# Performance work log

Measured on AMD Instinct MI355X. Metric: run time of the kernel, lower is better.

Reference implementation:

```python
import jax, jax.numpy as jnp
import numpy as np

TOP_K = 2

def setup_inputs() -> dict:
    key = jax.random.key(0)
    k1, k2, k3, k4 = jax.random.split(key, 4)
    B, S, H, E, F = 2, 1024, 1024, 16, 1024
    hidden_states = jax.random.normal(k1, (B, S, H), dtype=jnp.float32)
    router_w = jax.random.normal(k2, (H, E), dtype=jnp.float32) * 0.02
    w_gate_up = jax.random.normal(k3, (E, H, 2 * F), dtype=jnp.float32) * 0.02
    w_down = jax.random.normal(k4, (E, F, H), dtype=jnp.float32) * 0.02
    return {"hidden_states": hidden_states, "router_w": router_w,
            "w_gate_up": w_gate_up, "w_down": w_down}

def reference(hidden_states, router_w, w_gate_up, w_down):
    B, S, H = hidden_states.shape
    E = router_w.shape[-1]
    flat = hidden_states.reshape(-1, H)                      # [T, H]
    T = flat.shape[0]
    # Routing: topk_then_softmax (default softmax_order)
    logits = flat @ router_w                                 # [T, E]
    top_vals, top_idx = jax.lax.top_k(logits, TOP_K)         # [T, K]
    routing_weights = jax.nn.softmax(top_vals, axis=-1)      # [T, K]
    # Scatter routing weights into a dense combine matrix [T, E]
    combine = jnp.zeros((T, E), dtype=flat.dtype)
    combine = combine.at[jnp.arange(T)[:, None], top_idx].add(routing_weights)
    # Fused expert FFN (per _FusedExpertTemplate, act_fn = SiLU-gated)
    gu = jnp.einsum('th,ehf->etf', flat, w_gate_up)          # [E, T, 2F]
    gate, up = jnp.split(gu, 2, axis=-1)
    gated = jax.nn.silu(gate) * up                           # [E, T, F]
    expert_out = jnp.einsum('etf,efh->eth', gated, w_down)   # [E, T, H]
    out = jnp.einsum('eth,te->th', expert_out, combine)      # [T, H]
    return out.reshape(B, S, H)
```

## Files before the change

### kernel.cpp

```cpp
#include <hip/hip_runtime.h>

#define T_TOK 2048
#define H_DIM 1024
#define E_NUM 16
#define F_DIM 1024

typedef unsigned short u16;
typedef unsigned int u32;
typedef short s16x8 __attribute__((ext_vector_type(8)));
typedef float f32x4 __attribute__((ext_vector_type(4)));

__device__ __forceinline__ float b2f(u16 v) { return __uint_as_float(((u32)v) << 16); }
__device__ __forceinline__ u16 f2b(float f) {
  u32 u = __float_as_uint(f);
  return (u16)((u + 0x7fffu + ((u >> 16) & 1u)) >> 16);
}

__global__ void router_kernel(const float* __restrict__ hidden, const float* __restrict__ rw,
                              int* __restrict__ counts, int* __restrict__ routing_e,
                              float* __restrict__ routing_w) {
  int t = blockIdx.x;
  int lane = threadIdx.x;
  const float* xrow = hidden + (size_t)t * H_DIM;
  float acc[E_NUM];
#pragma unroll
  for (int e = 0; e < E_NUM; ++e) acc[e] = 0.f;
  for (int j = 0; j < H_DIM / 64; ++j) {
    int h = j * 64 + lane;
    float x = xrow[h];
    const float* wr = rw + h * E_NUM;
#pragma unroll
    for (int e = 0; e < E_NUM; ++e) acc[e] += x * wr[e];
  }
#pragma unroll
  for (int e = 0; e < E_NUM; ++e) {
    acc[e] += __shfl_xor(acc[e], 32, 64);
    acc[e] += __shfl_xor(acc[e], 16, 64);
    acc[e] += __shfl_xor(acc[e], 8, 64);
    acc[e] += __shfl_xor(acc[e], 4, 64);
    acc[e] += __shfl_xor(acc[e], 2, 64);
    acc[e] += __shfl_xor(acc[e], 1, 64);
  }
  if (lane == 0) {
    float v0 = -1e30f, v1 = -1e30f;
    int i0 = 0, i1 = 0;
#pragma unroll
    for (int e = 0; e < E_NUM; ++e) {
      float v = acc[e];
      if (v > v0) { v1 = v0; i1 = i0; v0 = v; i0 = e; }
      else if (v > v1) { v1 = v; i1 = e; }
    }
    float p0 = 1.f / (1.f + __expf(v1 - v0));
    routing_e[2 * t] = i0;
    routing_e[2 * t + 1] = i1;
    routing_w[2 * t] = p0;
    routing_w[2 * t + 1] = 1.f - p0;
    atomicAdd(&counts[i0], 1);
    atomicAdd(&counts[i1], 1);
  }
}

__global__ void scatter_kernel(const int* __restrict__ counts, int* __restrict__ offsets,
                               const int* __restrict__ routing_e, const float* __restrict__ routing_w,
                               int* __restrict__ token_of_slot, float* __restrict__ slot_w) {
  __shared__ int offs[E_NUM];
  __shared__ int cur[E_NUM];
  int tid = threadIdx.x;
  if (tid == 0) {
    int s = 0;
    for (int e = 0; e < E_NUM; ++e) { offs[e] = s; s += counts[e]; }
  }
  __syncthreads();
  if (tid < E_NUM) { offsets[tid] = offs[tid]; cur[tid] = offs[tid]; }
  __syncthreads();
  for (int i = tid; i < 2 * T_TOK; i += 256) {
    int e = routing_e[i];
    int pos = atomicAdd(&cur[e], 1);
    token_of_slot[pos] = i >> 1;
    slot_w[pos] = routing_w[i];
  }
}

struct f8v { float4 a, b; };

__device__ __forceinline__ void stage_w_pair(u32* __restrict__ B, int kp, int n0,
                                             const f8v& ev, const f8v& od) {
  const float* pe = (const float*)&ev;
  const float* po = (const float*)&od;
  int g0 = kp >> 2, w = kp & 3;
#pragma unroll
  for (int i = 0; i < 8; ++i) {
    int n = n0 + i;
    u32 word = (u32)f2b(pe[i]) | ((u32)f2b(po[i]) << 16);
    B[n * 16 + (((g0 ^ (n >> 3) ^ n) & 3) << 2) + w] = word;
  }
}

__device__ __forceinline__ s16x8 read_bfrag(const u32* __restrict__ B, int n, int q) {
  return *(const s16x8*)&B[n * 16 + (((q ^ (n >> 3) ^ n) & 3) << 2)];
}

__device__ __forceinline__ void split_pack(const float* __restrict__ p, uint4& hh, uint4& ll) {
  u16 h[8], l[8];
#pragma unroll
  for (int i = 0; i < 8; ++i) {
    h[i] = f2b(p[i]);
    l[i] = f2b(p[i] - b2f(h[i]));
  }
  hh.x = (u32)h[0] | ((u32)h[1] << 16);
  hh.y = (u32)h[2] | ((u32)h[3] << 16);
  hh.z = (u32)h[4] | ((u32)h[5] << 16);
  hh.w = (u32)h[6] | ((u32)h[7] << 16);
  ll.x = (u32)l[0] | ((u32)l[1] << 16);
  ll.y = (u32)l[2] | ((u32)l[3] << 16);
  ll.z = (u32)l[4] | ((u32)l[5] << 16);
  ll.w = (u32)l[6] | ((u32)l[7] << 16);
}

#define MFMA(a, b, c) __builtin_amdgcn_mfma_f32_16x16x32_bf16(a, b, c, 0, 0, 0)

__global__ __launch_bounds__(256, 2) void moe_gemm1(
    const float* __restrict__ hidden, const float* __restrict__ wgu,
    const int* __restrict__ token_of_slot, const int* __restrict__ counts,
    const int* __restrict__ offsets, float* __restrict__ act) {
  const int e = blockIdx.z;
  const int cnt = counts[e];
  const int m0 = blockIdx.y * 64;
  if (m0 >= cnt) return;
  const int off = offsets[e];
  const int f0 = blockIdx.x * 128;

  __shared__ u16 Xh[64][40];
  __shared__ u16 Xl[64][40];
  __shared__ u32 Bg[128 * 16];
  __shared__ u32 Bu[128 * 16];

  const int tid = threadIdx.x;
  const int lane = tid & 63;
  const int wave = tid >> 6;
  const int q = lane >> 4, ln = lane & 15;
  const int mb = (wave & 1) * 32, nb = (wave >> 1) * 64;

  const int xr = tid >> 2, xc = (tid & 3) * 8;
  const int tok = (m0 + xr < cnt) ? token_of_slot[off + m0 + xr] : 0;
  const float* xsrc = hidden + (size_t)tok * H_DIM + xc;

  const int kp = tid >> 4, n0 = (tid & 15) * 8;
  const float* wbase = wgu + (size_t)e * H_DIM * 2048;
  const float* wg0 = wbase + (size_t)(2 * kp) * 2048 + f0 + n0;
  const float* wu0 = wg0 + 1024;

  f32x4 zero = {0.f, 0.f, 0.f, 0.f};
  f32x4 accg[2][4], accu[2][4];
#pragma unroll
  for (int i = 0; i < 2; ++i)
#pragma unroll
    for (int j = 0; j < 4; ++j) { accg[i][j] = zero; accu[i][j] = zero; }

  for (int k0 = 0; k0 < H_DIM; k0 += 32) {
    float4 xa = *(const float4*)(xsrc + k0);
    float4 xb = *(const float4*)(xsrc + k0 + 4);
    size_t wofs = (size_t)k0 * 2048;
    f8v ge, go, ue, uo;
    ge.a = *(const float4*)(wg0 + wofs);
    ge.b = *(const float4*)(wg0 + wofs + 4);
    go.a = *(const float4*)(wg0 + wofs + 2048);
    go.b = *(const float4*)(wg0 + wofs + 2052);
    ue.a = *(const float4*)(wu0 + wofs);
    ue.b = *(const float4*)(wu0 + wofs + 4);
    uo.a = *(const float4*)(wu0 + wofs + 2048);
    uo.b = *(const float4*)(wu0 + wofs + 2052);
    __syncthreads();
    float xv[8] = {xa.x, xa.y, xa.z, xa.w, xb.x, xb.y, xb.z, xb.w};
    uint4 hh, ll;
    split_pack(xv, hh, ll);
    *(uint4*)&Xh[xr][xc] = hh;
    *(uint4*)&Xl[xr][xc] = ll;
    stage_w_pair(Bg, kp, n0, ge, go);
    stage_w_pair(Bu, kp, n0, ue, uo);
    __syncthreads();

    s16x8 ah[2], al[2];
    ah[0] = *(const s16x8*)&Xh[mb + ln][q * 8];
    ah[1] = *(const s16x8*)&Xh[mb + 16 + ln][q * 8];
    al[0] = *(const s16x8*)&Xl[mb + ln][q * 8];
    al[1] = *(const s16x8*)&Xl[mb + 16 + ln][q * 8];
#pragma unroll
    for (int j = 0; j < 4; ++j) {
      s16x8 bg = read_bfrag(Bg, nb + j * 16 + ln, q);
      s16x8 bu = read_bfrag(Bu, nb + j * 16 + ln, q);
#pragma unroll
      for (int i = 0; i < 2; ++i) {
        accg[i][j] = MFMA(ah[i], bg, accg[i][j]);
        accg[i][j] = MFMA(al[i], bg, accg[i][j]);
        accu[i][j] = MFMA(ah[i], bu, accu[i][j]);
        accu[i][j] = MFMA(al[i], bu, accu[i][j]);
      }
    }
  }

#pragma unroll
  for (int i = 0; i < 2; ++i) {
#pragma unroll
    for (int r = 0; r < 4; ++r) {
      int row = mb + i * 16 + q * 4 + r;
      if (m0 + row < cnt) {
        float* arow = act + (size_t)(off + m0 + row) * F_DIM + f0 + nb + ln;
#pragma unroll
        for (int j = 0; j < 4; ++j) {
          float g = accg[i][j][r], u = accu[i][j][r];
          arow[j * 16] = g * (1.f / (1.f + __expf(-g))) * u;
        }
      }
    }
  }
}

__global__ __launch_bounds__(256, 2) void moe_gemm2(
    const float* __restrict__ act, const float* __restrict__ wd,
    const int* __restrict__ token_of_slot, const float* __restrict__ slot_w,
    const int* __restrict__ counts, const int* __restrict__ offsets,
    float* __restrict__ out) {
  const int e = blockIdx.z;
  const int cnt = counts[e];
  const int m0 = blockIdx.y * 64;
  if (m0 >= cnt) return;
  const int off = offsets[e];
  const int h0 = blockIdx.x * 128;

  __shared__ u16 Ah[64][40];
  __shared__ u16 Al[64][40];
  __shared__ u32 Bd[128 * 16];

  const int tid = threadIdx.x;
  const int lane = tid & 63;
  const int wave = tid >> 6;
  const int q = lane >> 4, ln = lane & 15;
  const int mb = (wave & 1) * 32, nb = (wave >> 1) * 64;

  const int xr = tid >> 2, xc = (tid & 3) * 8;
  const int gs = (m0 + xr < cnt) ? (off + m0 + xr) : 0;
  const float* asrc = act + (size_t)gs * F_DIM + xc;

  const int kp = tid >> 4, n0 = (tid & 15) * 8;
  const float* wd0 = wd + (size_t)e * F_DIM * H_DIM + (size_t)(2 * kp) * H_DIM + h0 + n0;

  f32x4 zero = {0.f, 0.f, 0.f, 0.f};
  f32x4 acc[2][4];
#pragma unroll
  for (int i = 0; i < 2; ++i)
#pragma unroll
    for (int j = 0; j < 4; ++j) acc[i][j] = zero;

  for (int k0 = 0; k0 < F_DIM; k0 += 32) {
    float4 aa = *(const float4*)(asrc + k0);
    float4 ab = *(const float4*)(asrc + k0 + 4);
    size_t wofs = (size_t)k0 * H_DIM;
    f8v de, dd;
    de.a = *(const float4*)(wd0 + wofs);
    de.b = *(const float4*)(wd0 + wofs + 4);
    dd.a = *(const float4*)(wd0 + wofs + 1024);
    dd.b = *(const float4*)(wd0 + wofs + 1028);
    __syncthreads();
    float av[8] = {aa.x, aa.y, aa.z, aa.w, ab.x, ab.y, ab.z, ab.w};
    uint4 hh, ll;
    split_pack(av, hh, ll);
    *(uint4*)&Ah[xr][xc] = hh;
    *(uint4*)&Al[xr][xc] = ll;
    stage_w_pair(Bd, kp, n0, de, dd);
    __syncthreads();
    s16x8 ah[2], al[2];
    ah[0] = *(const s16x8*)&Ah[mb + ln][q * 8];
    ah[1] = *(const s16x8*)&Ah[mb + 16 + ln][q * 8];
    al[0] = *(const s16x8*)&Al[mb + ln][q * 8];
    al[1] = *(const s16x8*)&Al[mb + 16 + ln][q * 8];
#pragma unroll
    for (int j = 0; j < 4; ++j) {
      s16x8 bf = read_bfrag(Bd, nb + j * 16 + ln, q);
#pragma unroll
      for (int i = 0; i < 2; ++i) {
        acc[i][j] = MFMA(ah[i], bf, acc[i][j]);
        acc[i][j] = MFMA(al[i], bf, acc[i][j]);
      }
    }
  }
#pragma unroll
  for (int i = 0; i < 2; ++i) {
#pragma unroll
    for (int r = 0; r < 4; ++r) {
      int row = mb + i * 16 + q * 4 + r;
      if (m0 + row < cnt) {
        int slot = off + m0 + row;
        int tok = token_of_slot[slot];
        float wgt = slot_w[slot];
        float* orow = out + (size_t)tok * H_DIM + h0 + nb + ln;
#pragma unroll
        for (int j = 0; j < 4; ++j) atomicAdd(&orow[j * 16], wgt * acc[i][j][r]);
      }
    }
  }
}

extern "C" void kernel_launch(void* const* d_in, const int* in_sizes, int n_in,
                              void* d_out, int out_size, void* d_ws, size_t ws_size,
                              hipStream_t stream) {
  const float* hidden = (const float*)d_in[0];
  const float* rw = (const float*)d_in[1];
  const float* wgu = (const float*)d_in[2];
  const float* wd = (const float*)d_in[3];
  float* out = (float*)d_out;
  char* ws = (char*)d_ws;

  int* counts = (int*)(ws);
  int* offsets = (int*)(ws + 256);
  int* routing_e = (int*)(ws + 1024);
  float* routing_w = (float*)(ws + 17408);
  int* token_of_slot = (int*)(ws + 33792);
  float* slot_w = (float*)(ws + 50176);
  float* act = (float*)(ws + 131072);

  hipMemsetAsync(counts, 0, 64, stream);
  hipMemsetAsync(out, 0, (size_t)out_size * sizeof(float), stream);
  router_kernel<<<dim3(T_TOK), dim3(64), 0, stream>>>(hidden, rw, counts, routing_e, routing_w);
  scatter_kernel<<<dim3(1), dim3(256), 0, stream>>>(counts, offsets, routing_e, routing_w,
                                                    token_of_slot, slot_w);
  moe_gemm1<<<dim3(8, 32, E_NUM), dim3(256), 0, stream>>>(hidden, wgu, token_of_slot, counts,
                                                          offsets, act);
  moe_gemm2<<<dim3(8, 32, E_NUM), dim3(256), 0, stream>>>(act, wd, token_of_slot, slot_w, counts,
                                                          offsets, out);
}
```

Before: 433.6 us.

## Pre-transpose weights to bf16 and stream GEMM tiles via global_load_lds

Adds pre-passes that split hidden states into bf16 hi/lo arrays and transpose both expert weight tensors into K-contiguous bf16 layouts in workspace. New GEMM kernels then load tiles directly into swizzled LDS with global_load_lds, with no in-loop conversion. The intermediate activation is now stored in bf16, and GEMM2 drops the lo-part correction for it, which cuts traffic and MFMA count but lowers precision. The cost is a full read and write of about 200 MB of weights on every call. The old path is kept as a fallback when the workspace is too small.

```diff
diff --git a/kernel.cpp b/kernel.cpp
--- a/kernel.cpp
+++ b/kernel.cpp
@@ -15,6 +15,15 @@
   u32 u = __float_as_uint(f);
   return (u16)((u + 0x7fffu + ((u >> 16) & 1u)) >> 16);
 }
+
+typedef const __attribute__((address_space(1))) unsigned int ga_u32;
+typedef __attribute__((address_space(3))) unsigned int ls_u32;
+__device__ __forceinline__ void glds16(const void* g, void* l) {
+  __builtin_amdgcn_global_load_lds((ga_u32*)(unsigned long long)g,
+                                   (ls_u32*)(unsigned long long)l, 16, 0, 0);
+}
+
+#define MFMA(a, b, c) __builtin_amdgcn_mfma_f32_16x16x32_bf16(a, b, c, 0, 0, 0)
 
 __global__ void router_kernel(const float* __restrict__ hidden, const float* __restrict__ rw,
                               int* __restrict__ counts, int* __restrict__ routing_e,
@@ -81,25 +90,249 @@
   }
 }
 
+__global__ void split_hidden(const float* __restrict__ h, u16* __restrict__ xh,
+                             u16* __restrict__ xl) {
+  int idx = (blockIdx.x * 256 + threadIdx.x) * 8;
+  float4 a = *(const float4*)(h + idx);
+  float4 b = *(const float4*)(h + idx + 4);
+  float p[8] = {a.x, a.y, a.z, a.w, b.x, b.y, b.z, b.w};
+  u16 hh[8], ll[8];
+#pragma unroll
+  for (int i = 0; i < 8; ++i) {
+    hh[i] = f2b(p[i]);
+    ll[i] = f2b(p[i] - b2f(hh[i]));
+  }
+  uint4 ph, pl;
+  ph.x = (u32)hh[0] | ((u32)hh[1] << 16); ph.y = (u32)hh[2] | ((u32)hh[3] << 16);
+  ph.z = (u32)hh[4] | ((u32)hh[5] << 16); ph.w = (u32)hh[6] | ((u32)hh[7] << 16);
+  pl.x = (u32)ll[0] | ((u32)ll[1] << 16); pl.y = (u32)ll[2] | ((u32)ll[3] << 16);
+  pl.z = (u32)ll[4] | ((u32)ll[5] << 16); pl.w = (u32)ll[6] | ((u32)ll[7] << 16);
+  *(uint4*)(xh + idx) = ph;
+  *(uint4*)(xl + idx) = pl;
+}
+
+__global__ void transpose_f32_bf16(const float* __restrict__ src, u16* __restrict__ dst,
+                                   int R, int C) {
+  int b = blockIdx.z;
+  int c0 = blockIdx.x * 64, r0 = blockIdx.y * 64;
+  const float* s = src + (size_t)b * R * C;
+  u16* d = dst + (size_t)b * R * C;
+  __shared__ float tile[64][65];
+  int t = threadIdx.x;
+  int row = t >> 2, cc = (t & 3) * 16;
+#pragma unroll
+  for (int i = 0; i < 4; ++i) {
+    float4 v = *(const float4*)(s + (size_t)(r0 + row) * C + c0 + cc + i * 4);
+    tile[row][cc + i * 4 + 0] = v.x;
+    tile[row][cc + i * 4 + 1] = v.y;
+    tile[row][cc + i * 4 + 2] = v.z;
+    tile[row][cc + i * 4 + 3] = v.w;
+  }
+  __syncthreads();
+  int oc = t >> 2, rr = (t & 3) * 16;
+  u16 o[16];
+#pragma unroll
+  for (int j = 0; j < 16; ++j) o[j] = f2b(tile[rr + j][oc]);
+  uint4 p0, p1;
+  p0.x = (u32)o[0] | ((u32)o[1] << 16);  p0.y = (u32)o[2] | ((u32)o[3] << 16);
+  p0.z = (u32)o[4] | ((u32)o[5] << 16);  p0.w = (u32)o[6] | ((u32)o[7] << 16);
+  p1.x = (u32)o[8] | ((u32)o[9] << 16);  p1.y = (u32)o[10] | ((u32)o[11] << 16);
+  p1.z = (u32)o[12] | ((u32)o[13] << 16); p1.w = (u32)o[14] | ((u32)o[15] << 16);
+  u16* drow = d + (size_t)(c0 + oc) * R + r0 + rr;
+  *(uint4*)drow = p0;
+  *(uint4*)(drow + 8) = p1;
+}
+
+__device__ __forceinline__ int swz(int r) { return ((r & 3) ^ ((r >> 2) & 3)) & 3; }
+
+__global__ __launch_bounds__(256, 2) void moe_gemm1_fast(
+    const u16* __restrict__ xh, const u16* __restrict__ xl, const u16* __restrict__ wgu_t,
+    const int* __restrict__ token_of_slot, const int* __restrict__ counts,
+    const int* __restrict__ offsets, u16* __restrict__ act) {
+  const int e = blockIdx.z, cnt = counts[e];
+  const int m0 = blockIdx.y * 64;
+  if (m0 >= cnt) return;
+  const int off = offsets[e];
+  const int f0 = blockIdx.x * 128;
+
+  __shared__ u16 Xh[64 * 32], Xl[64 * 32], Bg[128 * 32], Bu[128 * 32];
+
+  const int tid = threadIdx.x, lane = tid & 63, w = tid >> 6;
+  const int q = lane >> 4, ln = lane & 15;
+  const int mb = (w & 1) * 32, nb = (w >> 1) * 64;
+
+  const int lr = lane >> 2, lc = lane & 3;
+  int ar = w * 16 + lr;
+  int tok = token_of_slot[(m0 + ar < cnt) ? (off + m0 + ar) : off];
+  int ac = (lc ^ swz(ar)) & 3;
+  const u16* gxh = xh + (size_t)tok * H_DIM + ac * 8;
+  const u16* gxl = xl + (size_t)tok * H_DIM + ac * 8;
+  u16* dxh = &Xh[w * 512];
+  u16* dxl = &Xl[w * 512];
+  int br0 = w * 32 + lr, br1 = br0 + 16;
+  int bc0 = (lc ^ swz(br0)) & 3, bc1 = (lc ^ swz(br1)) & 3;
+  const u16* wg_base = wgu_t + ((size_t)e * 2048 + f0) * H_DIM;
+  const u16* gbg0 = wg_base + (size_t)br0 * H_DIM + bc0 * 8;
+  const u16* gbg1 = wg_base + (size_t)br1 * H_DIM + bc1 * 8;
+  const u16* gbu0 = gbg0 + (size_t)1024 * H_DIM;
+  const u16* gbu1 = gbg1 + (size_t)1024 * H_DIM;
+  u16* dbg0 = &Bg[w * 1024];
+  u16* dbg1 = &Bg[w * 1024 + 512];
+  u16* dbu0 = &Bu[w * 1024];
+  u16* dbu1 = &Bu[w * 1024 + 512];
+
+  f32x4 zero = {0.f, 0.f, 0.f, 0.f};
+  f32x4 accg[2][4], accu[2][4];
+#pragma unroll
+  for (int i = 0; i < 2; ++i)
+#pragma unroll
+    for (int j = 0; j < 4; ++j) { accg[i][j] = zero; accu[i][j] = zero; }
+
+  for (int k0 = 0; k0 < H_DIM; k0 += 32) {
+    glds16(gxh + k0, dxh);
+    glds16(gxl + k0, dxl);
+    glds16(gbg0 + k0, dbg0);
+    glds16(gbg1 + k0, dbg1);
+    glds16(gbu0 + k0, dbu0);
+    glds16(gbu1 + k0, dbu1);
+    __syncthreads();
+
+    s16x8 ah[2], al[2];
+#pragma unroll
+    for (int i = 0; i < 2; ++i) {
+      int m = mb + i * 16 + ln;
+      int p = (q ^ swz(m)) & 3;
+      ah[i] = *(const s16x8*)&Xh[m * 32 + p * 8];
+      al[i] = *(const s16x8*)&Xl[m * 32 + p * 8];
+    }
+#pragma unroll
+    for (int j = 0; j < 4; ++j) {
+      int n = nb + j * 16 + ln;
+      int p = (q ^ swz(n)) & 3;
+      s16x8 bg = *(const s16x8*)&Bg[n * 32 + p * 8];
+      s16x8 bu = *(const s16x8*)&Bu[n * 32 + p * 8];
+#pragma unroll
+      for (int i = 0; i < 2; ++i) {
+        accg[i][j] = MFMA(ah[i], bg, accg[i][j]);
+        accg[i][j] = MFMA(al[i], bg, accg[i][j]);
+        accu[i][j] = MFMA(ah[i], bu, accu[i][j]);
+        accu[i][j] = MFMA(al[i], bu, accu[i][j]);
+      }
+    }
+    __syncthreads();
+  }
+
+#pragma unroll
+  for (int i = 0; i < 2; ++i) {
+#pragma unroll
+    for (int r = 0; r < 4; ++r) {
+      int row = mb + i * 16 + q * 4 + r;
+      if (m0 + row < cnt) {
+        u16* arow = act + (size_t)(off + m0 + row) * F_DIM + f0 + nb + ln;
+#pragma unroll
+        for (int j = 0; j < 4; ++j) {
+          float g = accg[i][j][r], u = accu[i][j][r];
+          arow[j * 16] = f2b(g * (1.f / (1.f + __expf(-g))) * u);
+        }
+      }
+    }
+  }
+}
+
+__global__ __launch_bounds__(256, 2) void moe_gemm2_fast(
+    const u16* __restrict__ act, const u16* __restrict__ wd_t,
+    const int* __restrict__ token_of_slot, const float* __restrict__ slot_w,
+    const int* __restrict__ counts, const int* __restrict__ offsets,
+    float* __restrict__ out) {
+  const int e = blockIdx.z, cnt = counts[e];
+  const int m0 = blockIdx.y * 64;
+  if (m0 >= cnt) return;
+  const int off = offsets[e];
+  const int h0 = blockIdx.x * 128;
+
+  __shared__ u16 As[64 * 32], Bd[128 * 32];
+
+  const int tid = threadIdx.x, lane = tid & 63, w = tid >> 6;
+  const int q = lane >> 4, ln = lane & 15;
+  const int mb = (w & 1) * 32, nb = (w >> 1) * 64;
+
+  const int lr = lane >> 2, lc = lane & 3;
+  int ar = w * 16 + lr;
+  int asl = (m0 + ar < cnt) ? (off + m0 + ar) : off;
+  int ac = (lc ^ swz(ar)) & 3;
+  const u16* ga = act + (size_t)asl * F_DIM + ac * 8;
+  u16* da = &As[w * 512];
+  int br0 = w * 32 + lr, br1 = br0 + 16;
+  int bc0 = (lc ^ swz(br0)) & 3, bc1 = (lc ^ swz(br1)) & 3;
+  const u16* wd_base = wd_t + ((size_t)e * 1024 + h0) * F_DIM;
+  const u16* gb0 = wd_base + (size_t)br0 * F_DIM + bc0 * 8;
+  const u16* gb1 = wd_base + (size_t)br1 * F_DIM + bc1 * 8;
+  u16* db0 = &Bd[w * 1024];
+  u16* db1 = &Bd[w * 1024 + 512];
+
+  f32x4 zero = {0.f, 0.f, 0.f, 0.f};
+  f32x4 acc[2][4];
+#pragma unroll
+  for (int i = 0; i < 2; ++i)
+#pragma unroll
+    for (int j = 0; j < 4; ++j) acc[i][j] = zero;
+
+  for (int k0 = 0; k0 < F_DIM; k0 += 32) {
+    glds16(ga + k0, da);
+    glds16(gb0 + k0, db0);
+    glds16(gb1 + k0, db1);
+    __syncthreads();
+    s16x8 af[2];
+#pragma unroll
+    for (int i = 0; i < 2; ++i) {
+      int m = mb + i * 16 + ln;
+      int p = (q ^ swz(m)) & 3;
+      af[i] = *(const s16x8*)&As[m * 32 + p * 8];
+    }
+#pragma unroll
+    for (int j = 0; j < 4; ++j) {
+      int n = nb + j * 16 + ln;
+      int p = (q ^ swz(n)) & 3;
+      s16x8 bf = *(const s16x8*)&Bd[n * 32 + p * 8];
+      acc[0][j] = MFMA(af[0], bf, acc[0][j]);
+      acc[1][j] = MFMA(af[1], bf, acc[1][j]);
+    }
+    __syncthreads();
+  }
+#pragma unroll
+  for (int i = 0; i < 2; ++i) {
+#pragma unroll
+    for (int r = 0; r < 4; ++r) {
+      int row = mb + i * 16 + q * 4 + r;
+      if (m0 + row < cnt) {
+        int slot = off + m0 + row;
+        int tok = token_of_slot[slot];
+        float wgt = slot_w[slot];
+        float* orow = out + (size_t)tok * H_DIM + h0 + nb + ln;
+#pragma unroll
+        for (int j = 0; j < 4; ++j) atomicAdd(&orow[j * 16], wgt * acc[i][j][r]);
+      }
+    }
+  }
+}
+
 struct f8v { float4 a, b; };
 
 __device__ __forceinline__ void stage_w_pair(u32* __restrict__ B, int kp, int n0,
                                              const f8v& ev, const f8v& od) {
   const float* pe = (const float*)&ev;
   const float* po = (const float*)&od;
-  int g0 = kp >> 2, w = kp & 3;
+  int g0 = kp >> 2, wv = kp & 3;
 #pragma unroll
   for (int i = 0; i < 8; ++i) {
     int n = n0 + i;
     u32 word = (u32)f2b(pe[i]) | ((u32)f2b(po[i]) << 16);
-    B[n * 16 + (((g0 ^ (n >> 3) ^ n) & 3) << 2) + w] = word;
-  }
-}
-
+    B[n * 16 + (((g0 ^ (n >> 3) ^ n) & 3) << 2) + wv] = word;
+  }
+}
 __device__ __forceinline__ s16x8 read_bfrag(const u32* __restrict__ B, int n, int q) {
   return *(const s16x8*)&B[n * 16 + (((q ^ (n >> 3) ^ n) & 3) << 2)];
 }
-
 __device__ __forceinline__ void split_pack(const float* __restrict__ p, uint4& hh, uint4& ll) {
   u16 h[8], l[8];
 #pragma unroll
@@ -107,56 +340,41 @@
     h[i] = f2b(p[i]);
     l[i] = f2b(p[i] - b2f(h[i]));
   }
-  hh.x = (u32)h[0] | ((u32)h[1] << 16);
-  hh.y = (u32)h[2] | ((u32)h[3] << 16);
-  hh.z = (u32)h[4] | ((u32)h[5] << 16);
-  hh.w = (u32)h[6] | ((u32)h[7] << 16);
-  ll.x = (u32)l[0] | ((u32)l[1] << 16);
-  ll.y = (u32)l[2] | ((u32)l[3] << 16);
-  ll.z = (u32)l[4] | ((u32)l[5] << 16);
-  ll.w = (u32)l[6] | ((u32)l[7] << 16);
-}
-
-#define MFMA(a, b, c) __builtin_amdgcn_mfma_f32_16x16x32_bf16(a, b, c, 0, 0, 0)
-
-__global__ __launch_bounds__(256, 2) void moe_gemm1(
+  hh.x = (u32)h[0] | ((u32)h[1] << 16); hh.y = (u32)h[2] | ((u32)h[3] << 16);
+  hh.z = (u32)h[4] | ((u32)h[5] << 16); hh.w = (u32)h[6] | ((u32)h[7] << 16);
+  ll.x = (u32)l[0] | ((u32)l[1] << 16); ll.y = (u32)l[2] | ((u32)l[3] << 16);
+  ll.z = (u32)l[4] | ((u32)l[5] << 16); ll.w = (u32)l[6] | ((u32)l[7] << 16);
+}
+
+__global__ __launch_bounds__(256, 2) void moe_gemm1_fb(
     const float* __restrict__ hidden, const float* __restrict__ wgu,
     const int* __restrict__ token_of_slot, const int* __restrict__ counts,
     const int* __restrict__ offsets, float* __restrict__ act) {
-  const int e = blockIdx.z;
-  const int cnt = counts[e];
+  const int e = blockIdx.z, cnt = counts[e];
   const int m0 = blockIdx.y * 64;
   if (m0 >= cnt) return;
   const int off = offsets[e];
   const int f0 = blockIdx.x * 128;
-
   __shared__ u16 Xh[64][40];
   __shared__ u16 Xl[64][40];
   __shared__ u32 Bg[128 * 16];
   __shared__ u32 Bu[128 * 16];
-
-  const int tid = threadIdx.x;
-  const int lane = tid & 63;
-  const int wave = tid >> 6;
+  const int tid = threadIdx.x, lane = tid & 63, wave = tid >> 6;
   const int q = lane >> 4, ln = lane & 15;
   const int mb = (wave & 1) * 32, nb = (wave >> 1) * 64;
-
   const int xr = tid >> 2, xc = (tid & 3) * 8;
   const int tok = (m0 + xr < cnt) ? token_of_slot[off + m0 + xr] : 0;
   const float* xsrc = hidden + (size_t)tok * H_DIM + xc;
-
   const int kp = tid >> 4, n0 = (tid & 15) * 8;
   const float* wbase = wgu + (size_t)e * H_DIM * 2048;
   const float* wg0 = wbase + (size_t)(2 * kp) * 2048 + f0 + n0;
   const float* wu0 = wg0 + 1024;
-
   f32x4 zero = {0.f, 0.f, 0.f, 0.f};
   f32x4 accg[2][4], accu[2][4];
 #pragma unroll
   for (int i = 0; i < 2; ++i)
 #pragma unroll
     for (int j = 0; j < 4; ++j) { accg[i][j] = zero; accu[i][j] = zero; }
-
   for (int k0 = 0; k0 < H_DIM; k0 += 32) {
     float4 xa = *(const float4*)(xsrc + k0);
     float4 xb = *(const float4*)(xsrc + k0 + 4);
@@ -179,7 +397,6 @@
     stage_w_pair(Bg, kp, n0, ge, go);
     stage_w_pair(Bu, kp, n0, ue, uo);
     __syncthreads();
-
     s16x8 ah[2], al[2];
     ah[0] = *(const s16x8*)&Xh[mb + ln][q * 8];
     ah[1] = *(const s16x8*)&Xh[mb + 16 + ln][q * 8];
@@ -198,7 +415,6 @@
       }
     }
   }
-
 #pragma unroll
   for (int i = 0; i < 2; ++i) {
 #pragma unroll
@@ -216,42 +432,33 @@
   }
 }
 
-__global__ __launch_bounds__(256, 2) void moe_gemm2(
+__global__ __launch_bounds__(256, 2) void moe_gemm2_fb(
     const float* __restrict__ act, const float* __restrict__ wd,
     const int* __restrict__ token_of_slot, const float* __restrict__ slot_w,
     const int* __restrict__ counts, const int* __restrict__ offsets,
     float* __restrict__ out) {
-  const int e = blockIdx.z;
-  const int cnt = counts[e];
+  const int e = blockIdx.z, cnt = counts[e];
   const int m0 = blockIdx.y * 64;
   if (m0 >= cnt) return;
   const int off = offsets[e];
   const int h0 = blockIdx.x * 128;
-
   __shared__ u16 Ah[64][40];
   __shared__ u16 Al[64][40];
   __shared__ u32 Bd[128 * 16];
-
-  const int tid = threadIdx.x;
-  const int lane = tid & 63;
-  const int wave = tid >> 6;
+  const int tid = threadIdx.x, lane = tid & 63, wave = tid >> 6;
   const int q = lane >> 4, ln = lane & 15;
   const int mb = (wave & 1) * 32, nb = (wave >> 1) * 64;
-
   const int xr = tid >> 2, xc = (tid & 3) * 8;
   const int gs = (m0 + xr < cnt) ? (off + m0 + xr) : 0;
   const float* asrc = act + (size_t)gs * F_DIM + xc;
-
   const int kp = tid >> 4, n0 = (tid & 15) * 8;
   const float* wd0 = wd + (size_t)e * F_DIM * H_DIM + (size_t)(2 * kp) * H_DIM + h0 + n0;
-
   f32x4 zero = {0.f, 0.f, 0.f, 0.f};
   f32x4 acc[2][4];
 #pragma unroll
   for (int i = 0; i < 2; ++i)
 #pragma unroll
     for (int j = 0; j < 4; ++j) acc[i][j] = zero;
-
   for (int k0 = 0; k0 < F_DIM; k0 += 32) {
     float4 aa = *(const float4*)(asrc + k0);
     float4 ab = *(const float4*)(asrc + k0 + 4);
@@ -317,15 +524,33 @@
   float* routing_w = (float*)(ws + 17408);
   int* token_of_slot = (int*)(ws + 33792);
   float* slot_w = (float*)(ws + 50176);
-  float* act = (float*)(ws + 131072);
 
   hipMemsetAsync(counts, 0, 64, stream);
   hipMemsetAsync(out, 0, (size_t)out_size * sizeof(float), stream);
   router_kernel<<<dim3(T_TOK), dim3(64), 0, stream>>>(hidden, rw, counts, routing_e, routing_w);
   scatter_kernel<<<dim3(1), dim3(256), 0, stream>>>(counts, offsets, routing_e, routing_w,
                                                     token_of_slot, slot_w);
-  moe_gemm1<<<dim3(8, 32, E_NUM), dim3(256), 0, stream>>>(hidden, wgu, token_of_slot, counts,
-                                                          offsets, act);
-  moe_gemm2<<<dim3(8, 32, E_NUM), dim3(256), 0, stream>>>(act, wd, token_of_slot, slot_w, counts,
-                                                          offsets, out);
-}
+
+  const size_t NEED = 117571584ull;
+  if (ws_size >= NEED) {
+    u16* act = (u16*)(ws + 131072);
+    u16* xh = (u16*)(ws + 8519680);
+    u16* xl = (u16*)(ws + 12713984);
+    u16* wgu_t = (u16*)(ws + 16908288);
+    u16* wd_t = (u16*)(ws + 84017152);
+
+    split_hidden<<<dim3(1024), dim3(256), 0, stream>>>(hidden, xh, xl);
+    transpose_f32_bf16<<<dim3(32, 16, E_NUM), dim3(256), 0, stream>>>(wgu, wgu_t, 1024, 2048);
+    transpose_f32_bf16<<<dim3(16, 16, E_NUM), dim3(256), 0, stream>>>(wd, wd_t, 1024, 1024);
+    moe_gemm1_fast<<<dim3(8, 32, E_NUM), dim3(256), 0, stream>>>(xh, xl, wgu_t, token_of_slot,
+                                                                 counts, offsets, act);
+    moe_gemm2_fast<<<dim3(8, 32, E_NUM), dim3(256), 0, stream>>>(act, wd_t, token_of_slot, slot_w,
+                                                                 counts, offsets, out);
+  } else {
+    float* act = (float*)(ws + 131072);
+    moe_gemm1_fb<<<dim3(8, 32, E_NUM), dim3(256), 0, stream>>>(hidden, wgu, token_of_slot, counts,
+                                                               offsets, act);
+    moe_gemm2_fb<<<dim3(8, 32, E_NUM), dim3(256), 0, stream>>>(act, wd, token_of_slot, slot_w,
+                                                               counts, offsets, out);
+  }
+}
```

Result: slower. 465.9 us (+7.4%).
